# Kernel tuning notes

Measured on AMD Instinct MI355X. Metric: run time of the kernel, lower is better.

Reference implementation:

```python
import jax, jax.numpy as jnp
import numpy as np

N_HEAD = 16
MASK_PENALTY = 10000.0


def setup_inputs() -> dict:
    key = jax.random.key(0)
    k1, k2, k3 = jax.random.split(key, 3)
    B, S, D = 2, 2048, 1024
    x = jax.random.normal(k1, (B, S, D), dtype=jnp.float32)
    w_attn = jax.random.normal(k2, (D, 3 * D), dtype=jnp.float32) * 0.02
    b_attn = jnp.zeros((3 * D,), dtype=jnp.float32)
    w_proj = jax.random.normal(k3, (D, D), dtype=jnp.float32) * 0.02
    b_proj = jnp.zeros((D,), dtype=jnp.float32)
    return {"x": x, "w_attn": w_attn, "b_attn": b_attn, "w_proj": w_proj, "b_proj": b_proj}


def _split_heads(t, n_head):
    B, S, D = t.shape
    return t.reshape(B, S, n_head, D // n_head).transpose(0, 2, 1, 3)  # [B,H,S,dh]


def reference(x, w_attn, b_attn, w_proj, b_proj):
    B, S, D = x.shape
    qkv = x @ w_attn + b_attn  # fused QKV conv1d: [B,S,3D]
    q, k, v = jnp.split(qkv, 3, axis=2)
    q = _split_heads(q, N_HEAD)
    k = _split_heads(k, N_HEAD)
    v = _split_heads(v, N_HEAD)
    dh = D // N_HEAD
    w = jnp.einsum("bhqd,bhkd->bhqk", q, k) / jnp.sqrt(jnp.asarray(dh, dtype=q.dtype))
    # GPT-2 additive causal mask: w*b - 10000*(1-b)
    i = jnp.arange(S)[:, None]
    j = jnp.arange(S)[None, :]
    b = (i >= j).astype(w.dtype)  # nd == ns here
    w = w * b - MASK_PENALTY * (1.0 - b)
    w = jax.nn.softmax(w, axis=-1)
    a = jnp.einsum("bhqk,bhkd->bhqd", w, v)  # [B,H,S,dh]
    a = a.transpose(0, 2, 1, 3).reshape(B, S, D)  # merge heads
    return a @ w_proj + b_proj
```

## Files before the change

### kernel.cpp

```cpp
#include <hip/hip_runtime.h>
#include <hip/hip_bf16.h>


typedef short short8 __attribute__((ext_vector_type(8)));
typedef float f32x4 __attribute__((ext_vector_type(4)));

__device__ __forceinline__ unsigned short f2b(float f) {
    unsigned int x;
    __builtin_memcpy(&x, &f, 4);
    unsigned int r = x + 0x7FFF + ((x >> 16) & 1);
    return (unsigned short)(r >> 16);
}

__device__ __forceinline__ unsigned int pk2(float a, float b) {
    __hip_bfloat162 h = __float22bfloat162_rn(make_float2(a, b));
    unsigned int u;
    __builtin_memcpy(&u, &h, 4);
    return u;
}

__device__ __forceinline__ void load_lds16(const unsigned short* g, unsigned short* l) {
    __builtin_amdgcn_global_load_lds(
        (const __attribute__((address_space(1))) unsigned int*)g,
        (__attribute__((address_space(3))) unsigned int*)l, 16, 0, 0);
}

__global__ __launch_bounds__(256) void prep(const float* __restrict__ x, unsigned int* __restrict__ xb,
                                            const float* __restrict__ wA, unsigned short* __restrict__ wtA,
                                            const float* __restrict__ wP, unsigned short* __restrict__ wtP) {
    const int bx = blockIdx.x, tid = threadIdx.x;
    if (bx < 4096) {
        int i = (bx * 256 + tid) * 4;
        float4 f = *(const float4*)(x + i);
        uint2 p;
        p.x = (unsigned int)f2b(f.x) | ((unsigned int)f2b(f.y) << 16);
        p.y = (unsigned int)f2b(f.z) | ((unsigned int)f2b(f.w) << 16);
        *(uint2*)(xb + i / 2) = p;
        return;
    }
    __shared__ unsigned short t[32][33];
    const float* in;
    unsigned short* out;
    int R, C, gx, gy;
    if (bx < 7168) { int i = bx - 4096; gx = i % 96; gy = i / 96; in = wA; out = wtA; R = 1024; C = 3072; }
    else           { int i = bx - 7168; gx = i % 32; gy = i / 32; in = wP; out = wtP; R = 1024; C = 1024; }
    const int tx = tid & 31, ty = tid >> 5;
    const int c0 = gx * 32, r0 = gy * 32;
#pragma unroll
    for (int i = 0; i < 4; i++)
        t[ty + i * 8][tx] = f2b(in[(r0 + ty + i * 8) * C + c0 + tx]);
    __syncthreads();
#pragma unroll
    for (int i = 0; i < 4; i++)
        out[(c0 + ty + i * 8) * R + r0 + tx] = t[tx][ty + i * 8];
}

__global__ __launch_bounds__(256) void qkv_gemm(const unsigned short* __restrict__ X,
                                                const unsigned short* __restrict__ WT,
                                                const float* __restrict__ bias,
                                                unsigned short* __restrict__ Qo,
                                                unsigned short* __restrict__ Ko,
                                                unsigned short* __restrict__ Vt) {
    __shared__ __align__(16) unsigned short SM[16384];
    unsigned short* As = SM;
    unsigned short* Bs = SM + 8192;
    const int tid = threadIdx.x;
    const int w = tid >> 6, l = tid & 63, l15 = l & 15, quad = l >> 4;
    const int wr = w >> 1, wc = w & 1;
    const int m0 = blockIdx.y * 128, n0 = blockIdx.x * 128;

    const int sr = w * 16 + (l >> 2);
    const int gch = (l & 3) ^ ((l >> 3) & 3);
    const unsigned short* Asrc = X + (size_t)(m0 + sr) * 1024 + gch * 8;
    const unsigned short* Bsrc = WT + (size_t)(n0 + sr) * 1024 + gch * 8;
    const int rswz = (l15 >> 1) & 3;

    f32x4 acc[4][4];
#pragma unroll
    for (int mt = 0; mt < 4; mt++)
#pragma unroll
        for (int nt = 0; nt < 4; nt++) acc[mt][nt] = (f32x4){0.f, 0.f, 0.f, 0.f};

    load_lds16(Asrc, &As[tid * 8]);
    load_lds16(Asrc + 65536, &As[2048 + tid * 8]);
    load_lds16(Bsrc, &Bs[tid * 8]);
    load_lds16(Bsrc + 65536, &Bs[2048 + tid * 8]);

    for (int k0 = 0; k0 < 1024; k0 += 32) {
        const int c = (k0 >> 5) & 1;
        __syncthreads();
        if (k0 + 32 < 1024) {
            const int pc = 1 - c;
            load_lds16(Asrc + k0 + 32, &As[pc * 4096 + tid * 8]);
            load_lds16(Asrc + 65536 + k0 + 32, &As[pc * 4096 + 2048 + tid * 8]);
            load_lds16(Bsrc + k0 + 32, &Bs[pc * 4096 + tid * 8]);
            load_lds16(Bsrc + 65536 + k0 + 32, &Bs[pc * 4096 + 2048 + tid * 8]);
        }

        short8 af[4], bfr[4];
#pragma unroll
        for (int mt = 0; mt < 4; mt++)
            af[mt] = *(const short8*)&As[c * 4096 + (wr * 64 + mt * 16 + l15) * 32 + ((quad ^ rswz) * 8)];
#pragma unroll
        for (int nt = 0; nt < 4; nt++)
            bfr[nt] = *(const short8*)&Bs[c * 4096 + (wc * 64 + nt * 16 + l15) * 32 + ((quad ^ rswz) * 8)];
#pragma unroll
        for (int mt = 0; mt < 4; mt++)
#pragma unroll
            for (int nt = 0; nt < 4; nt++)
                acc[mt][nt] = __builtin_amdgcn_mfma_f32_16x16x32_bf16(af[mt], bfr[nt], acc[mt][nt], 0, 0, 0);
    }

    const int which = n0 >> 10;
    const int c0 = n0 & 1023;
    float bv[4];
#pragma unroll
    for (int nt = 0; nt < 4; nt++) bv[nt] = bias[n0 + wc * 64 + nt * 16 + l15];

    if (which < 2) {
        const float scale = (which == 1) ? 0.125f : 1.0f;
        unsigned short* dst = (which == 0) ? Qo : Ko;
#pragma unroll
        for (int mt = 0; mt < 4; mt++)
#pragma unroll
            for (int nt = 0; nt < 4; nt++)
#pragma unroll
                for (int r = 0; r < 4; r++) {
                    int mg = m0 + wr * 64 + mt * 16 + quad * 4 + r;
                    int cg = c0 + wc * 64 + nt * 16 + l15;
                    float v = (acc[mt][nt][r] + bv[nt]) * scale;
                    int h = cg >> 6, d = cg & 63;
                    dst[(((size_t)(mg >> 11) * 16 + h) * 2048 + (mg & 2047)) * 64 + d] = f2b(v);
                }
    } else {
        const int b = m0 >> 11, sbase = m0 & 2047, h0 = c0 >> 6;
#pragma unroll
        for (int p = 0; p < 2; p++) {
            __syncthreads();
            if (wc == p) {
#pragma unroll
                for (int mt = 0; mt < 4; mt++)
#pragma unroll
                    for (int nt = 0; nt < 4; nt++)
#pragma unroll
                        for (int r = 0; r < 4; r++) {
                            float v = acc[mt][nt][r] + bv[nt];
                            int d = nt * 16 + l15;
                            int mloc = wr * 64 + mt * 16 + quad * 4 + r;
                            SM[d * 128 + (((mloc >> 4) ^ (d & 7)) << 4) + (mloc & 15)] = f2b(v);
                        }
            }
            __syncthreads();
            const int d = tid >> 2, q4 = tid & 3;
            size_t gb = ((size_t)((b * 16 + h0 + p) * 64 + d)) * 2048 + sbase + q4 * 32;
#pragma unroll
            for (int half = 0; half < 2; half++) {
                int mc = q4 * 2 + half;
                const uint4* s = (const uint4*)&SM[d * 128 + ((mc ^ (d & 7)) << 4)];
                *(uint4*)(Vt + gb + half * 16) = s[0];
                *(uint4*)(Vt + gb + half * 16 + 8) = s[1];
            }
        }
    }
}

__global__ __launch_bounds__(256) void attn_k(const unsigned short* __restrict__ Q,
                                              const unsigned short* __restrict__ K,
                                              const unsigned short* __restrict__ Vt,
                                              unsigned short* __restrict__ Om) {
    __shared__ __align__(16) unsigned short SM[20480];
    unsigned short* Ks0 = SM;
    unsigned short* Vts0 = SM + 8192;
    unsigned short* QP = SM + 16384;

    const int tid = threadIdx.x;
    const int w = tid >> 6, l = tid & 63, l15 = l & 15, quad = l >> 4;
    const int wq = w >> 1, ws = w & 1;
    const int bid = blockIdx.x;
    const int qt = 31 - (bid >> 5);
    const int hb = bid & 31;
    const int q0 = qt * 64;
    const unsigned short* Qb = Q + (size_t)hb * 131072;
    const unsigned short* Kb = K + (size_t)hb * 131072;
    const unsigned short* Vb = Vt + (size_t)hb * 131072;

    const int sr = w * 8 + (l >> 3);
    const int gch = (l & 7) ^ (l >> 3);
    const int swz7 = l15 & 7;

    load_lds16(Qb + (q0 + sr) * 64 + gch * 8, &QP[tid * 8]);
    load_lds16(Qb + (q0 + 32 + sr) * 64 + gch * 8, &QP[2048 + tid * 8]);
    load_lds16(Kb + sr * 64 + gch * 8, &Ks0[tid * 8]);
    load_lds16(Kb + (32 + sr) * 64 + gch * 8, &Ks0[2048 + tid * 8]);
    load_lds16(Vb + sr * 2048 + gch * 8, &Vts0[tid * 8]);
    load_lds16(Vb + (32 + sr) * 2048 + gch * 8, &Vts0[2048 + tid * 8]);
    __syncthreads();

    short8 qf[2][2];
#pragma unroll
    for (int qnt = 0; qnt < 2; qnt++)
#pragma unroll
        for (int ks = 0; ks < 2; ks++)
            qf[qnt][ks] = *(const short8*)&QP[(wq * 32 + qnt * 16 + l15) * 64 + (((ks * 4 + quad) ^ swz7) << 3)];

    short8 ones;
#pragma unroll
    for (int j = 0; j < 8; j++) ones[j] = (short)0x3F80;

    f32x4 o[2][4], lacc[2];
#pragma unroll
    for (int pmt = 0; pmt < 2; pmt++) {
        lacc[pmt] = (f32x4){0.f, 0.f, 0.f, 0.f};
#pragma unroll
        for (int dnt = 0; dnt < 4; dnt++) o[pmt][dnt] = (f32x4){0.f, 0.f, 0.f, 0.f};
    }

    for (int kt = 0; kt <= qt; kt++) {
        const int c = kt & 1;
        const unsigned short* Ksc = Ks0 + c * 4096;
        const unsigned short* Vtsc = Vts0 + c * 4096;
        __syncthreads();
        if (kt < qt) {
            const int kn = (kt + 1) * 64, pc = 1 - c;
            load_lds16(Kb + (kn + sr) * 64 + gch * 8, &Ks0[pc * 4096 + tid * 8]);
            load_lds16(Kb + (kn + 32 + sr) * 64 + gch * 8, &Ks0[pc * 4096 + 2048 + tid * 8]);
            load_lds16(Vb + sr * 2048 + kn + gch * 8, &Vts0[pc * 4096 + tid * 8]);
            load_lds16(Vb + (32 + sr) * 2048 + kn + gch * 8, &Vts0[pc * 4096 + 2048 + tid * 8]);
        }

        f32x4 sa[2][2];
#pragma unroll
        for (int smt = 0; smt < 2; smt++)
#pragma unroll
            for (int qnt = 0; qnt < 2; qnt++) sa[smt][qnt] = (f32x4){0.f, 0.f, 0.f, 0.f};
#pragma unroll
        for (int ks = 0; ks < 2; ks++) {
            short8 kf[2];
#pragma unroll
            for (int smt = 0; smt < 2; smt++)
                kf[smt] = *(const short8*)&Ksc[(ws * 32 + smt * 16 + l15) * 64 + (((ks * 4 + quad) ^ swz7) << 3)];
#pragma unroll
            for (int smt = 0; smt < 2; smt++)
#pragma unroll
                for (int qnt = 0; qnt < 2; qnt++)
                    sa[smt][qnt] = __builtin_amdgcn_mfma_f32_16x16x32_bf16(kf[smt], qf[qnt][ks], sa[smt][qnt], 0, 0, 0);
        }

        float pv[2][2][4];
        if (kt == qt) {
#pragma unroll
            for (int smt = 0; smt < 2; smt++)
#pragma unroll
                for (int qnt = 0; qnt < 2; qnt++)
#pragma unroll
                    for (int r = 0; r < 4; r++) {
                        int cg = kt * 64 + ws * 32 + smt * 16 + quad * 4 + r;
                        int rg = q0 + wq * 32 + qnt * 16 + l15;
                        pv[smt][qnt][r] = (cg <= rg) ? __expf(sa[smt][qnt][r]) : 0.f;
                    }
        } else {
#pragma unroll
            for (int smt = 0; smt < 2; smt++)
#pragma unroll
                for (int qnt = 0; qnt < 2; qnt++)
#pragma unroll
                    for (int r = 0; r < 4; r++)
                        pv[smt][qnt][r] = __expf(sa[smt][qnt][r]);
        }

#pragma unroll
        for (int smt = 0; smt < 2; smt++)
#pragma unroll
            for (int qnt = 0; qnt < 2; qnt++) {
                int q = wq * 32 + qnt * 16 + l15;
                int sb = ws * 32 + smt * 16 + quad * 4;
                int ch = (sb >> 3) ^ (q & 7);
                int a16 = q * 64 + (ch << 3) + (sb & 7);
                uint2 u;
                u.x = pk2(pv[smt][qnt][0], pv[smt][qnt][1]);
                u.y = pk2(pv[smt][qnt][2], pv[smt][qnt][3]);
                *(uint2*)&QP[a16] = u;
            }
        asm volatile("s_waitcnt lgkmcnt(0)" ::: "memory");

        short8 pf[2];
#pragma unroll
        for (int pmt = 0; pmt < 2; pmt++) {
            pf[pmt] = *(const short8*)&QP[(wq * 32 + pmt * 16 + l15) * 64 + (((ws * 4 + quad) ^ swz7) << 3)];
            lacc[pmt] = __builtin_amdgcn_mfma_f32_16x16x32_bf16(pf[pmt], ones, lacc[pmt], 0, 0, 0);
        }
#pragma unroll
        for (int dnt = 0; dnt < 4; dnt++) {
            short8 vf = *(const short8*)&Vtsc[(dnt * 16 + l15) * 64 + (((ws * 4 + quad) ^ swz7) << 3)];
#pragma unroll
            for (int pmt = 0; pmt < 2; pmt++)
                o[pmt][dnt] = __builtin_amdgcn_mfma_f32_16x16x32_bf16(pf[pmt], vf, o[pmt][dnt], 0, 0, 0);
        }
    }

    __syncthreads();
    float* red = (float*)SM;
    float* myp = red + (wq * 64 + l) * 41;
    if (ws == 1) {
#pragma unroll
        for (int pmt = 0; pmt < 2; pmt++) {
#pragma unroll
            for (int dnt = 0; dnt < 4; dnt++)
#pragma unroll
                for (int r = 0; r < 4; r++) myp[pmt * 16 + dnt * 4 + r] = o[pmt][dnt][r];
#pragma unroll
            for (int r = 0; r < 4; r++) myp[32 + pmt * 4 + r] = lacc[pmt][r];
        }
    }
    __syncthreads();
    if (ws == 0) {
        float inv[2][4];
#pragma unroll
        for (int pmt = 0; pmt < 2; pmt++)
#pragma unroll
            for (int r = 0; r < 4; r++)
                inv[pmt][r] = 1.0f / (lacc[pmt][r] + myp[32 + pmt * 4 + r]);
        const int b = hb >> 4, h = hb & 15;
#pragma unroll
        for (int pmt = 0; pmt < 2; pmt++)
#pragma unroll
            for (int dnt = 0; dnt < 4; dnt++)
#pragma unroll
                for (int r = 0; r < 4; r++) {
                    float val = (o[pmt][dnt][r] + myp[pmt * 16 + dnt * 4 + r]) * inv[pmt][r];
                    int sg = q0 + wq * 32 + pmt * 16 + quad * 4 + r;
                    int col = h * 64 + dnt * 16 + l15;
                    Om[((size_t)(b * 2048 + sg)) * 1024 + col] = f2b(val);
                }
    }
}

__global__ __launch_bounds__(256) void proj_gemm(const unsigned short* __restrict__ A,
                                                 const unsigned short* __restrict__ WT,
                                                 const float* __restrict__ bias,
                                                 float* __restrict__ out) {
    __shared__ __align__(16) unsigned short As[2][4096];
    __shared__ __align__(16) unsigned short Bs[2][2048];
    const int tid = threadIdx.x;
    const int w = tid >> 6, l = tid & 63, l15 = l & 15, quad = l >> 4;
    const int wr = w >> 1, wc = w & 1;
    const int m0 = blockIdx.y * 128, n0 = blockIdx.x * 64;

    const int sr = w * 16 + (l >> 2);
    const int gch = (l & 3) ^ ((l >> 3) & 3);
    const unsigned short* Asrc = A + (size_t)(m0 + sr) * 1024 + gch * 8;
    const unsigned short* Bsrc = WT + (size_t)(n0 + sr) * 1024 + gch * 8;
    const int rswz = (l15 >> 1) & 3;

    f32x4 acc[4][2];
#pragma unroll
    for (int mt = 0; mt < 4; mt++)
#pragma unroll
        for (int nt = 0; nt < 2; nt++) acc[mt][nt] = (f32x4){0.f, 0.f, 0.f, 0.f};

    load_lds16(Asrc, &As[0][tid * 8]);
    load_lds16(Asrc + 65536, &As[0][2048 + tid * 8]);
    load_lds16(Bsrc, &Bs[0][tid * 8]);

    for (int k0 = 0; k0 < 1024; k0 += 32) {
        const int c = (k0 >> 5) & 1;
        __syncthreads();
        if (k0 + 32 < 1024) {
            const int pc = 1 - c;
            load_lds16(Asrc + k0 + 32, &As[pc][tid * 8]);
            load_lds16(Asrc + 65536 + k0 + 32, &As[pc][2048 + tid * 8]);
            load_lds16(Bsrc + k0 + 32, &Bs[pc][tid * 8]);
        }

        short8 af[4], bfr[2];
#pragma unroll
        for (int mt = 0; mt < 4; mt++)
            af[mt] = *(const short8*)&As[c][(wr * 64 + mt * 16 + l15) * 32 + ((quad ^ rswz) * 8)];
#pragma unroll
        for (int nt = 0; nt < 2; nt++)
            bfr[nt] = *(const short8*)&Bs[c][(wc * 32 + nt * 16 + l15) * 32 + ((quad ^ rswz) * 8)];
#pragma unroll
        for (int mt = 0; mt < 4; mt++)
#pragma unroll
            for (int nt = 0; nt < 2; nt++)
                acc[mt][nt] = __builtin_amdgcn_mfma_f32_16x16x32_bf16(af[mt], bfr[nt], acc[mt][nt], 0, 0, 0);
    }

#pragma unroll
    for (int mt = 0; mt < 4; mt++)
#pragma unroll
        for (int nt = 0; nt < 2; nt++)
#pragma unroll
            for (int r = 0; r < 4; r++) {
                int mg = m0 + wr * 64 + mt * 16 + quad * 4 + r;
                int ng = n0 + wc * 32 + nt * 16 + l15;
                out[(size_t)mg * 1024 + ng] = acc[mt][nt][r] + bias[ng];
            }
}

extern "C" void kernel_launch(void* const* d_in, const int* in_sizes, int n_in,
                              void* d_out, int out_size, void* d_ws, size_t ws_size,
                              hipStream_t stream) {
    (void)in_sizes; (void)n_in; (void)out_size; (void)ws_size;
    const float* x      = (const float*)d_in[0];
    const float* w_attn = (const float*)d_in[1];
    const float* b_attn = (const float*)d_in[2];
    const float* w_proj = (const float*)d_in[3];
    const float* b_proj = (const float*)d_in[4];
    float* out = (float*)d_out;
    unsigned short* ws = (unsigned short*)d_ws;

    unsigned short* wtA  = ws;
    unsigned short* wtP  = wtA + 3145728;
    unsigned short* Qw   = wtP + 1048576;
    unsigned short* Kw   = Qw + 4194304;
    unsigned short* Vtw  = Kw + 4194304;
    unsigned short* XbOm = Vtw + 4194304;

    prep<<<8192, 256, 0, stream>>>(x, (unsigned int*)XbOm, w_attn, wtA, w_proj, wtP);
    qkv_gemm<<<dim3(24, 32), 256, 0, stream>>>(XbOm, wtA, b_attn, Qw, Kw, Vtw);
    attn_k<<<1024, 256, 0, stream>>>(Qw, Kw, Vtw, XbOm);
    proj_gemm<<<dim3(16, 32), 256, 0, stream>>>(XbOm, wtP, b_proj, out);
}
```

Measured before the change: 172.1 us.

## Restructure QKV GEMM into 256x256 tiles with phased 8-wave pipeline

Rewrites the QKV projection GEMM to use 256x256 output tiles with 512 threads (8 waves), K-step of 64, and a four-phase schedule where each quarter of the next tile is staged into LDS while MFMAs run on the current quarter. It adds explicit s_barrier/vmcnt waits and s_setprio around the MFMA bursts, and adjusts the V-transpose epilogue for the larger tile. The aim is more data reuse per LDS load and better overlap of global loads with matrix math, at the cost of 128KB LDS, higher register pressure, and only 192 blocks for the grid.

New measurement: 171.3 us. Within noise of the previous version (-0.5%).

```diff
diff --git a/kernel.cpp b/kernel.cpp
--- a/kernel.cpp
+++ b/kernel.cpp
@@ -55,110 +55,155 @@
         out[(c0 + ty + i * 8) * R + r0 + tx] = t[tx][ty + i * 8];
 }
 
-__global__ __launch_bounds__(256) void qkv_gemm(const unsigned short* __restrict__ X,
-                                                const unsigned short* __restrict__ WT,
-                                                const float* __restrict__ bias,
-                                                unsigned short* __restrict__ Qo,
-                                                unsigned short* __restrict__ Ko,
-                                                unsigned short* __restrict__ Vt) {
-    __shared__ __align__(16) unsigned short SM[16384];
-    unsigned short* As = SM;
-    unsigned short* Bs = SM + 8192;
+
+#define QKV_PHASE(MH, NH, LAF, LBF, STAGE, WAITOP)                                      \
+  {                                                                                     \
+    if (LAF) {                                                                          \
+      const unsigned short* Ab_ = Al + (c * 2 + (MH)) * 8192 + (wr * 64 + l15) * 64;    \
+      _Pragma("unroll") for (int mt = 0; mt < 4; ++mt)                                  \
+        _Pragma("unroll") for (int ks = 0; ks < 2; ++ks)                                \
+          af[mt][ks] = *(const short8*)(Ab_ + mt * 1024 + k_off[ks]);                   \
+    }                                                                                   \
+    if (LBF) {                                                                          \
+      const unsigned short* Bb_ = Bl + (c * 2 + (NH)) * 8192 + (wc * 32 + l15) * 64;    \
+      _Pragma("unroll") for (int nt = 0; nt < 2; ++nt)                                  \
+        _Pragma("unroll") for (int ks = 0; ks < 2; ++ks)                                \
+          bf[NH][nt][ks] = *(const short8*)(Bb_ + nt * 1024 + k_off[ks]);               \
+    }                                                                                   \
+    STAGE;                                                                              \
+    asm volatile("s_barrier" ::: "memory");                                             \
+    asm volatile("s_waitcnt lgkmcnt(0)" ::: "memory");                                  \
+    __builtin_amdgcn_sched_barrier(0);                                                  \
+    __builtin_amdgcn_s_setprio(1);                                                      \
+    _Pragma("unroll") for (int ks = 0; ks < 2; ++ks)                                    \
+      _Pragma("unroll") for (int mt = 0; mt < 4; ++mt)                                  \
+        _Pragma("unroll") for (int nt = 0; nt < 2; ++nt)                                \
+          acc[(MH) * 4 + mt][(NH) * 2 + nt] = __builtin_amdgcn_mfma_f32_16x16x32_bf16(  \
+              af[mt][ks], bf[NH][nt][ks], acc[(MH) * 4 + mt][(NH) * 2 + nt], 0, 0, 0);  \
+    __builtin_amdgcn_s_setprio(0);                                                      \
+    WAITOP;                                                                             \
+    asm volatile("s_barrier" ::: "memory");                                             \
+  }
+
+__global__ __launch_bounds__(512, 2) void qkv_gemm(const unsigned short* __restrict__ X,
+                                                   const unsigned short* __restrict__ WT,
+                                                   const float* __restrict__ bias,
+                                                   unsigned short* __restrict__ Qo,
+                                                   unsigned short* __restrict__ Ko,
+                                                   unsigned short* __restrict__ Vt) {
+    __shared__ __align__(16) unsigned short SM[65536];
+    unsigned short* Al = SM;
+    unsigned short* Bl = SM + 32768;
+
     const int tid = threadIdx.x;
     const int w = tid >> 6, l = tid & 63, l15 = l & 15, quad = l >> 4;
-    const int wr = w >> 1, wc = w & 1;
-    const int m0 = blockIdx.y * 128, n0 = blockIdx.x * 128;
-
-    const int sr = w * 16 + (l >> 2);
-    const int gch = (l & 3) ^ ((l >> 3) & 3);
-    const unsigned short* Asrc = X + (size_t)(m0 + sr) * 1024 + gch * 8;
-    const unsigned short* Bsrc = WT + (size_t)(n0 + sr) * 1024 + gch * 8;
-    const int rswz = (l15 >> 1) & 3;
-
-    f32x4 acc[4][4];
-#pragma unroll
-    for (int mt = 0; mt < 4; mt++)
-#pragma unroll
-        for (int nt = 0; nt < 4; nt++) acc[mt][nt] = (f32x4){0.f, 0.f, 0.f, 0.f};
-
-    load_lds16(Asrc, &As[tid * 8]);
-    load_lds16(Asrc + 65536, &As[2048 + tid * 8]);
-    load_lds16(Bsrc, &Bs[tid * 8]);
-    load_lds16(Bsrc + 65536, &Bs[2048 + tid * 8]);
-
-    for (int k0 = 0; k0 < 1024; k0 += 32) {
-        const int c = (k0 >> 5) & 1;
-        __syncthreads();
-        if (k0 + 32 < 1024) {
-            const int pc = 1 - c;
-            load_lds16(Asrc + k0 + 32, &As[pc * 4096 + tid * 8]);
-            load_lds16(Asrc + 65536 + k0 + 32, &As[pc * 4096 + 2048 + tid * 8]);
-            load_lds16(Bsrc + k0 + 32, &Bs[pc * 4096 + tid * 8]);
-            load_lds16(Bsrc + 65536 + k0 + 32, &Bs[pc * 4096 + 2048 + tid * 8]);
-        }
-
-        short8 af[4], bfr[4];
-#pragma unroll
-        for (int mt = 0; mt < 4; mt++)
-            af[mt] = *(const short8*)&As[c * 4096 + (wr * 64 + mt * 16 + l15) * 32 + ((quad ^ rswz) * 8)];
-#pragma unroll
-        for (int nt = 0; nt < 4; nt++)
-            bfr[nt] = *(const short8*)&Bs[c * 4096 + (wc * 64 + nt * 16 + l15) * 32 + ((quad ^ rswz) * 8)];
-#pragma unroll
-        for (int mt = 0; mt < 4; mt++)
-#pragma unroll
-            for (int nt = 0; nt < 4; nt++)
-                acc[mt][nt] = __builtin_amdgcn_mfma_f32_16x16x32_bf16(af[mt], bfr[nt], acc[mt][nt], 0, 0, 0);
+    const int wr = w >> 2, wc = w & 3;
+    const int m0 = blockIdx.y * 256, n0 = blockIdx.x * 256;
+
+    const int rl = tid >> 3;
+    const int ch = (tid & 7) ^ (rl & 7);
+    const unsigned short* Asrc = X + (size_t)m0 * 1024 + ch * 8;
+    const unsigned short* Bsrc = WT + (size_t)n0 * 1024 + ch * 8;
+
+    int k_off[2];
+#pragma unroll
+    for (int ks = 0; ks < 2; ++ks) k_off[ks] = (((ks * 4 + quad) ^ (l15 & 7)) << 3);
+
+    auto stageA = [&](int buf, int half, int k0) {
+#pragma unroll
+        for (int j = 0; j < 2; ++j)
+            load_lds16(Asrc + (size_t)(j * 128 + half * 64 + rl) * 1024 + k0,
+                       Al + (buf * 2 + half) * 8192 + j * 4096 + tid * 8);
+    };
+    auto stageB = [&](int buf, int grp, int k0) {
+#pragma unroll
+        for (int j = 0; j < 2; ++j) {
+            int idx = j * 64 + rl;
+            int r = (idx >> 5) * 64 + grp * 32 + (idx & 31);
+            load_lds16(Bsrc + (size_t)r * 1024 + k0,
+                       Bl + (buf * 2 + grp) * 8192 + j * 4096 + tid * 8);
+        }
+    };
+
+    f32x4 acc[8][4];
+#pragma unroll
+    for (int m8 = 0; m8 < 8; ++m8)
+#pragma unroll
+        for (int n4 = 0; n4 < 4; ++n4) acc[m8][n4] = (f32x4){0.f, 0.f, 0.f, 0.f};
+
+    short8 af[4][2], bf[2][2][2];
+
+    stageA(0, 0, 0);
+    stageB(0, 0, 0);
+    stageB(0, 1, 0);
+    stageA(0, 1, 0);
+    asm volatile("s_waitcnt vmcnt(4)" ::: "memory");
+    asm volatile("s_barrier" ::: "memory");
+
+#pragma unroll 1
+    for (int t = 0; t < 15; ++t) {
+        const int c = t & 1, nb = c ^ 1;
+        const int kn = (t + 1) * 64;
+        QKV_PHASE(0, 0, 1, 1, stageA(nb, 0, kn), asm volatile("s_waitcnt vmcnt(4)" ::: "memory"))
+        QKV_PHASE(0, 1, 0, 1, stageB(nb, 0, kn), asm volatile("s_waitcnt vmcnt(4)" ::: "memory"))
+        QKV_PHASE(1, 0, 1, 0, stageB(nb, 1, kn), )
+        QKV_PHASE(1, 1, 0, 0, stageA(nb, 1, kn), asm volatile("s_waitcnt vmcnt(4)" ::: "memory"))
+    }
+    {
+        const int c = 1;
+        QKV_PHASE(0, 0, 1, 1, , asm volatile("s_waitcnt vmcnt(2)" ::: "memory"))
+        QKV_PHASE(0, 1, 0, 1, , asm volatile("s_waitcnt vmcnt(0)" ::: "memory"))
+        QKV_PHASE(1, 0, 1, 0, , )
+        QKV_PHASE(1, 1, 0, 0, , )
     }
 
     const int which = n0 >> 10;
     const int c0 = n0 & 1023;
     float bv[4];
 #pragma unroll
-    for (int nt = 0; nt < 4; nt++) bv[nt] = bias[n0 + wc * 64 + nt * 16 + l15];
+    for (int n4 = 0; n4 < 4; ++n4) bv[n4] = bias[n0 + wc * 64 + n4 * 16 + l15];
 
     if (which < 2) {
         const float scale = (which == 1) ? 0.125f : 1.0f;
         unsigned short* dst = (which == 0) ? Qo : Ko;
-#pragma unroll
-        for (int mt = 0; mt < 4; mt++)
-#pragma unroll
-            for (int nt = 0; nt < 4; nt++)
-#pragma unroll
-                for (int r = 0; r < 4; r++) {
-                    int mg = m0 + wr * 64 + mt * 16 + quad * 4 + r;
-                    int cg = c0 + wc * 64 + nt * 16 + l15;
-                    float v = (acc[mt][nt][r] + bv[nt]) * scale;
-                    int h = cg >> 6, d = cg & 63;
+        const int h = (c0 + wc * 64) >> 6;
+#pragma unroll
+        for (int m8 = 0; m8 < 8; ++m8)
+#pragma unroll
+            for (int n4 = 0; n4 < 4; ++n4)
+#pragma unroll
+                for (int r = 0; r < 4; ++r) {
+                    int mg = m0 + wr * 128 + m8 * 16 + quad * 4 + r;
+                    int d = n4 * 16 + l15;
+                    float v = (acc[m8][n4][r] + bv[n4]) * scale;
                     dst[(((size_t)(mg >> 11) * 16 + h) * 2048 + (mg & 2047)) * 64 + d] = f2b(v);
                 }
     } else {
         const int b = m0 >> 11, sbase = m0 & 2047, h0 = c0 >> 6;
 #pragma unroll
-        for (int p = 0; p < 2; p++) {
-            __syncthreads();
-            if (wc == p) {
-#pragma unroll
-                for (int mt = 0; mt < 4; mt++)
-#pragma unroll
-                    for (int nt = 0; nt < 4; nt++)
-#pragma unroll
-                        for (int r = 0; r < 4; r++) {
-                            float v = acc[mt][nt][r] + bv[nt];
-                            int d = nt * 16 + l15;
-                            int mloc = wr * 64 + mt * 16 + quad * 4 + r;
-                            SM[d * 128 + (((mloc >> 4) ^ (d & 7)) << 4) + (mloc & 15)] = f2b(v);
+        for (int p = 0; p < 2; ++p) {
+            asm volatile("s_barrier" ::: "memory");
+            if (wr == p) {
+#pragma unroll
+                for (int m8 = 0; m8 < 8; ++m8)
+#pragma unroll
+                    for (int n4 = 0; n4 < 4; ++n4)
+#pragma unroll
+                        for (int r = 0; r < 4; ++r) {
+                            float v = acc[m8][n4][r] + bv[n4];
+                            int d = n4 * 16 + l15;
+                            int m = m8 * 16 + quad * 4 + r;
+                            SM[(wc * 64 + d) * 128 + ((((m >> 4) ^ (d & 7))) << 4) + (m & 15)] = f2b(v);
                         }
             }
             __syncthreads();
-            const int d = tid >> 2, q4 = tid & 3;
-            size_t gb = ((size_t)((b * 16 + h0 + p) * 64 + d)) * 2048 + sbase + q4 * 32;
-#pragma unroll
-            for (int half = 0; half < 2; half++) {
-                int mc = q4 * 2 + half;
-                const uint4* s = (const uint4*)&SM[d * 128 + ((mc ^ (d & 7)) << 4)];
-                *(uint4*)(Vt + gb + half * 16) = s[0];
-                *(uint4*)(Vt + gb + half * 16 + 8) = s[1];
+            const int d = (tid >> 3) & 63, mc = tid & 7;
+#pragma unroll
+            for (int q = 0; q < 4; ++q) {
+                const uint4* s = (const uint4*)&SM[(q * 64 + d) * 128 + ((mc ^ (d & 7)) << 4)];
+                size_t gb = ((size_t)((b * 16 + h0 + q) * 64 + d)) * 2048 + sbase + p * 128 + mc * 16;
+                *(uint4*)(Vt + gb) = s[0];
+                *(uint4*)(Vt + gb + 8) = s[1];
             }
         }
     }
@@ -274,8 +319,8 @@
             for (int qnt = 0; qnt < 2; qnt++) {
                 int q = wq * 32 + qnt * 16 + l15;
                 int sb = ws * 32 + smt * 16 + quad * 4;
-                int ch = (sb >> 3) ^ (q & 7);
-                int a16 = q * 64 + (ch << 3) + (sb & 7);
+                int chp = (sb >> 3) ^ (q & 7);
+                int a16 = q * 64 + (chp << 3) + (sb & 7);
                 uint2 u;
                 u.x = pk2(pv[smt][qnt][0], pv[smt][qnt][1]);
                 u.y = pk2(pv[smt][qnt][2], pv[smt][qnt][3]);
@@ -418,7 +463,7 @@
     unsigned short* XbOm = Vtw + 4194304;
 
     prep<<<8192, 256, 0, stream>>>(x, (unsigned int*)XbOm, w_attn, wtA, w_proj, wtP);
-    qkv_gemm<<<dim3(24, 32), 256, 0, stream>>>(XbOm, wtA, b_attn, Qw, Kw, Vtw);
+    qkv_gemm<<<dim3(12, 16), 512, 0, stream>>>(XbOm, wtA, b_attn, Qw, Kw, Vtw);
     attn_k<<<1024, 256, 0, stream>>>(Qw, Kw, Vtw, XbOm);
     proj_gemm<<<dim3(16, 32), 256, 0, stream>>>(XbOm, wtP, b_proj, out);
 }
```
